# Kernel tuning notes

Measured on AMD Instinct MI355X. Metric: run time of the kernel, lower is better.

Reference implementation:

```python
import jax, jax.numpy as jnp
import numpy as np

T, N, L_DIM, P_DIM = 8192, 4096, 64, 32
IN_DIM = 3 * L_DIM  # library = [identity, square, sin]
MIN_TEMP, ALPHA, REP_COEF = 0.01, 0.999, 0.1


def build_library(X):
    # (T, L) -> (T, 3L): concatenated library features
    return jnp.concatenate([X, X * X, jnp.sin(X)], axis=1)


def setup_inputs() -> dict:
    key = jax.random.key(0)
    k = jax.random.split(key, 8)
    u = jax.random.uniform(k[6], (P_DIM, IN_DIM), minval=1e-7, maxval=1.0)
    return {
        "X_tilde_t_batch": jax.random.normal(k[0], (T, L_DIM), jnp.float32),
        "X_train_t_batch": jax.random.normal(k[1], (T, N), jnp.float32),
        "Y_train_t_batch": jax.random.normal(k[2], (T, N), jnp.float32),
        "temp": jnp.ones((1,), jnp.float32),
        "phi_bar_t": jax.random.normal(k[3], (P_DIM, L_DIM), jnp.float32) * 0.01,
        # spectral radius ~0.9 so the 8192-step linear recurrence stays bounded
        "A_tilde": jax.random.normal(k[4], (L_DIM, L_DIM), jnp.float32) * (0.9 / np.sqrt(L_DIM)),
        "U_l": jax.random.normal(k[5], (N, L_DIM), jnp.float32) / np.sqrt(N),
        "logits": jax.random.normal(k[7], (P_DIM, IN_DIM), jnp.float32),
        "gumbel_g": -jnp.log(-jnp.log(u)),  # Gumbel(0,1) noise, precomputed
    }


def reference(X_tilde_t_batch, X_train_t_batch, Y_train_t_batch, temp,
              phi_bar_t, A_tilde, U_l, logits, gumbel_g):
    # --- GumbelSelector (train=True) ---
    X_mod = build_library(X_tilde_t_batch)                           # (T, 3L)
    new_temp = jnp.maximum(MIN_TEMP, temp[0] * ALPHA)
    soft = jax.nn.softmax((logits + gumbel_g) / new_temp, axis=-1)   # (P, 3L)
    X_sel = X_mod @ soft.T                                           # (T, P) -- computed but unused downstream, as in source
    selected_idx = jnp.argmax(logits, axis=-1)                       # (P,)
    probs = jax.nn.softmax(logits, axis=-1)
    l0_pen = REP_COEF * jnp.sum(jnp.max(probs, axis=-1))             # computed, unused (as in source)

    # --- reconstruction_error: sequential linear state-space recurrence ---
    x0 = X_train_t_batch[0]                                          # (N,)  first column of X_train_batch
    xh0 = U_l.T @ x0                                                 # (L,)  projected initial state
    phi_bar = phi_bar_t.T                                            # (L, P)

    def step(xh, _):
        mod_sel = jnp.take(xh, selected_idx, mode='clip')            # (P,) irregular gather (clip matches jit take)
        xh = A_tilde @ xh + phi_bar @ mod_sel                        # tiny matvecs
        return xh, xh

    _, xh_seq = jax.lax.scan(step, xh0, None, length=T)              # (T, L)
    X_rec = xh_seq @ U_l.T                                           # (T, N) == (U_r @ xh_seq.T).T with U_r = U_l
    # Frobenius norm is transpose-invariant, so compute in (T, N) layout
    err = jnp.linalg.norm(Y_train_t_batch - X_rec) / jnp.linalg.norm(Y_train_t_batch)
    return (X_rec, err, new_temp, selected_idx)
```

## Files before the change

kernel.cpp:

```cpp
#include <hip/hip_runtime.h>
#include <math.h>

#define T_DIM 8192
#define N_DIM 4096
#define L 64
#define P 32
#define IN_DIM 192
#define S_CHUNK 16
#define N_CHUNK (T_DIM / S_CHUNK)
#define LDST 68

using f32x4   = __attribute__((ext_vector_type(4))) float;
using bf16x8  = __attribute__((ext_vector_type(8))) short;
using ushort8 = __attribute__((ext_vector_type(8))) unsigned short;

__device__ __forceinline__ unsigned short f2bf(float x) {
  unsigned u = __float_as_uint(x);
  u += 0x7fffu + ((u >> 16) & 1u);
  return (unsigned short)(u >> 16);
}
__device__ __forceinline__ float bf2f(unsigned short h) {
  return __uint_as_float(((unsigned)h) << 16);
}

__device__ __forceinline__ bf16x8 ldfrag(const unsigned short* __restrict__ base,
                                         int tile16, int gb, int lg, int lr) {
  return *(const bf16x8*)(base + ((size_t)((tile16 * 16 + gb + lg) * 16 + lr)) * 8);
}

__global__ __launch_bounds__(64) void k_xh0_part(const float* __restrict__ U,
                                                 const float* __restrict__ Xtr,
                                                 float* __restrict__ part,
                                                 double* __restrict__ acc) {
  int b = blockIdx.x;
  int l = threadIdx.x;
  if (b == 0 && l < 2) acc[l] = 0.0;
  int n0 = b * 64;
  float s = 0.f;
  #pragma unroll 8
  for (int i = 0; i < 64; ++i) {
    float x = Xtr[n0 + i];
    s += U[(size_t)(n0 + i) * L + l] * x;
  }
  part[b * 64 + l] = s;
}

__global__ __launch_bounds__(256) void k_usplit(const float* __restrict__ U,
                                                unsigned short* __restrict__ upk) {
  int idx = blockIdx.x * 256 + threadIdx.x;
  int lr = idx & 15, g = (idx >> 4) & 15, nn16 = idx >> 8;
  int n = nn16 * 16 + lr;
  int k0 = (g & 7) * 8;
  float4 a = *(const float4*)(U + (size_t)n * L + k0);
  float4 b = *(const float4*)(U + (size_t)n * L + k0 + 4);
  ushort8 o;
  float v[8] = {a.x, a.y, a.z, a.w, b.x, b.y, b.z, b.w};
  #pragma unroll
  for (int j = 0; j < 8; ++j) {
    unsigned short h = f2bf(v[j]);
    o[j] = (g < 8) ? h : f2bf(v[j] - bf2f(h));
  }
  *(ushort8*)(upk + (size_t)idx * 8) = o;
}

__global__ __launch_bounds__(256, 1) void k_prep(const float* __restrict__ A_tilde,
                                                 const float* __restrict__ phi_bar_t,
                                                 const float* __restrict__ logits,
                                                 const float* __restrict__ temp,
                                                 const float* __restrict__ part,
                                                 float* __restrict__ Wm,
                                                 float* __restrict__ xh0,
                                                 float* __restrict__ out_tail) {
  __shared__ float buf[2][64 * LDST];
  __shared__ float sphi[P * L];
  __shared__ float spart[4 * 64];
  __shared__ int   sel_s[P];
  int tid = threadIdx.x;

  #pragma unroll
  for (int i = 0; i < 4; ++i) {
    int f = tid + 256 * i;
    int r = f >> 4, q = f & 15;
    float4 v = ((const float4*)A_tilde)[f];
    *(float4*)(buf[0] + r * LDST + q * 4) = v;
  }
  #pragma unroll
  for (int i = 0; i < 2; ++i) {
    int f = tid + 256 * i;
    ((float4*)sphi)[f] = ((const float4*)phi_bar_t)[f];
  }
  {
    int l = tid & 63, q = tid >> 6;
    float s = 0.f;
    #pragma unroll
    for (int i = 0; i < 16; ++i)
      s += part[(q * 16 + i) * 64 + l];
    spart[q * 64 + l] = s;
  }
  {
    int p = tid >> 3, d = tid & 7;
    const float* row = logits + p * IN_DIM;
    float best = -1e30f; int bk = 0;
    #pragma unroll
    for (int j = 0; j < 6; ++j) {
      int kb = (j * 8 + d) * 4;
      float4 v = *(const float4*)(row + kb);
      if (v.x > best) { best = v.x; bk = kb; }
      if (v.y > best) { best = v.y; bk = kb + 1; }
      if (v.z > best) { best = v.z; bk = kb + 2; }
      if (v.w > best) { best = v.w; bk = kb + 3; }
    }
    #pragma unroll
    for (int off = 4; off > 0; off >>= 1) {
      float vo = __shfl_down(best, off, 8);
      int   ko = __shfl_down(bk,   off, 8);
      if (vo > best || (vo == best && ko < bk)) { best = vo; bk = ko; }
    }
    if (d == 0) {
      sel_s[p] = bk;
      out_tail[2 + p] = (float)bk;
    }
  }
  if (tid == 255) out_tail[1] = fmaxf(0.01f, temp[0] * 0.999f);
  __syncthreads();

  if (tid < L) {
    #pragma unroll 4
    for (int p = 0; p < P; ++p) {
      int kk = sel_s[p]; if (kk > L - 1) kk = L - 1;
      buf[0][tid * LDST + kk] += sphi[p * L + tid];
    }
  } else if (tid < 128) {
    int l = tid - 64;
    xh0[l] = spart[l] + spart[64 + l] + spart[128 + l] + spart[192 + l];
  }
  __syncthreads();

  #pragma unroll
  for (int i = 0; i < 4; ++i) {
    int f = tid + 256 * i;
    int r = f >> 4, q = f & 15;
    *(float4*)(Wm + r * 64 + q * 4) = *(const float4*)(buf[0] + r * LDST + q * 4);
  }

  int r0 = (tid >> 4) << 2;
  int c0 = (tid & 15) << 2;
  int cur = 0;
  for (int j = 1; j <= 12; ++j) {
    const float* S = buf[cur];
    float* D = buf[cur ^ 1];
    float acc[4][4];
    #pragma unroll
    for (int i = 0; i < 4; ++i)
      #pragma unroll
      for (int c = 0; c < 4; ++c) acc[i][c] = 0.f;

    #pragma unroll
    for (int kb = 0; kb < 64; kb += 16) {
      float a[4][16];
      #pragma unroll
      for (int i = 0; i < 4; ++i)
        #pragma unroll
        for (int q = 0; q < 4; ++q) {
          float4 t4 = *(const float4*)(S + (r0 + i) * LDST + kb + q * 4);
          a[i][q * 4 + 0] = t4.x; a[i][q * 4 + 1] = t4.y;
          a[i][q * 4 + 2] = t4.z; a[i][q * 4 + 3] = t4.w;
        }
      #pragma unroll
      for (int kk = 0; kk < 16; ++kk) {
        float4 b4 = *(const float4*)(S + (kb + kk) * LDST + c0);
        #pragma unroll
        for (int i = 0; i < 4; ++i) {
          acc[i][0] += a[i][kk] * b4.x;
          acc[i][1] += a[i][kk] * b4.y;
          acc[i][2] += a[i][kk] * b4.z;
          acc[i][3] += a[i][kk] * b4.w;
        }
      }
    }
    #pragma unroll
    for (int i = 0; i < 4; ++i) {
      float4 o = {acc[i][0], acc[i][1], acc[i][2], acc[i][3]};
      *(float4*)(D + (r0 + i) * LDST + c0) = o;
      *(float4*)(Wm + j * 4096 + (r0 + i) * 64 + c0) = o;
    }
    __syncthreads();
    cur ^= 1;
  }
}

__global__ __launch_bounds__(64) void k_states(const float* __restrict__ Wm,
                                               const float* __restrict__ xh0,
                                               unsigned short* __restrict__ xpk) {
  __shared__ float sx[16 * LDST];
  int c = blockIdx.x;
  int l = threadIdx.x;
  float v = xh0[l];
  int e = c << 4;
  for (int j = 4; j <= 12; ++j) {
    if ((e >> j) & 1) {
      const float* W = Wm + j * 4096;
      float n0 = 0.f, n1 = 0.f, n2 = 0.f, n3 = 0.f;
      #pragma unroll
      for (int k = 0; k < 64; k += 4) {
        n0 += W[l * 64 + k]     * __shfl(v, k, 64);
        n1 += W[l * 64 + k + 1] * __shfl(v, k + 1, 64);
        n2 += W[l * 64 + k + 2] * __shfl(v, k + 2, 64);
        n3 += W[l * 64 + k + 3] * __shfl(v, k + 3, 64);
      }
      v = (n0 + n1) + (n2 + n3);
    }
  }
  float m[64];
  #pragma unroll
  for (int k = 0; k < 64; ++k) m[k] = Wm[l * 64 + k];
  for (int i = 0; i < S_CHUNK; ++i) {
    float n0 = 0.f, n1 = 0.f, n2 = 0.f, n3 = 0.f;
    #pragma unroll
    for (int k = 0; k < 64; k += 4) {
      n0 += m[k]     * __shfl(v, k, 64);
      n1 += m[k + 1] * __shfl(v, k + 1, 64);
      n2 += m[k + 2] * __shfl(v, k + 2, 64);
      n3 += m[k + 3] * __shfl(v, k + 3, 64);
    }
    v = (n0 + n1) + (n2 + n3);
    sx[i * LDST + l] = v;
  }
  __syncthreads();

  #pragma unroll
  for (int it = 0; it < 4; ++it) {
    int idx = l + 64 * it;
    int lr = idx & 15, g = idx >> 4;
    int k0 = (g & 7) * 8;
    float4 a = *(const float4*)(sx + lr * LDST + k0);
    float4 b = *(const float4*)(sx + lr * LDST + k0 + 4);
    float vv[8] = {a.x, a.y, a.z, a.w, b.x, b.y, b.z, b.w};
    ushort8 o;
    #pragma unroll
    for (int j = 0; j < 8; ++j) {
      unsigned short h = f2bf(vv[j]);
      o[j] = (g < 8) ? h : f2bf(vv[j] - bf2f(h));
    }
    *(ushort8*)(xpk + ((size_t)c * 256 + idx) * 8) = o;
  }
}

__global__ __launch_bounds__(256, 3) void k_xrec(const unsigned short* __restrict__ xpk,
                                                 const unsigned short* __restrict__ upk,
                                                 const float* __restrict__ Y,
                                                 float* __restrict__ Xrec,
                                                 double* __restrict__ acc_g) {
  __shared__ float red[512];

  int tid = threadIdx.x;
  int nt = blockIdx.x & 31, tt = blockIdx.x >> 5;
  int n0 = nt * 128, t0 = tt * 128;

  int l = tid & 63, wid = tid >> 6;
  int wr = wid >> 1, wc = wid & 1;
  int lr = l & 15, lg = l >> 4;

  int xt = (t0 >> 4) + wr * 4;
  int un = (n0 >> 4) + wc * 4;

  f32x4 acc[4][4];
  #pragma unroll
  for (int m = 0; m < 4; ++m)
    #pragma unroll
    for (int nf = 0; nf < 4; ++nf) acc[m][nf] = (f32x4){0.f, 0.f, 0.f, 0.f};

  bf16x8 af[4], bfr[4], bf2r[4];

  #pragma unroll
  for (int m = 0; m < 4; ++m)  af[m]   = ldfrag(xpk, xt + m, 0, lg, lr);
  #pragma unroll
  for (int nf = 0; nf < 4; ++nf) bfr[nf]  = ldfrag(upk, un + nf, 0, lg, lr);
  #pragma unroll
  for (int nf = 0; nf < 4; ++nf) bf2r[nf] = ldfrag(upk, un + nf, 8, lg, lr);
  #pragma unroll
  for (int m = 0; m < 4; ++m)
    #pragma unroll
    for (int nf = 0; nf < 4; ++nf)
      acc[m][nf] = __builtin_amdgcn_mfma_f32_16x16x32_bf16(bfr[nf], af[m], acc[m][nf], 0, 0, 0);
  #pragma unroll
  for (int m = 0; m < 4; ++m)
    #pragma unroll
    for (int nf = 0; nf < 4; ++nf)
      acc[m][nf] = __builtin_amdgcn_mfma_f32_16x16x32_bf16(bf2r[nf], af[m], acc[m][nf], 0, 0, 0);

  #pragma unroll
  for (int m = 0; m < 4; ++m)  af[m]   = ldfrag(xpk, xt + m, 4, lg, lr);
  #pragma unroll
  for (int nf = 0; nf < 4; ++nf) bfr[nf]  = ldfrag(upk, un + nf, 4, lg, lr);
  #pragma unroll
  for (int nf = 0; nf < 4; ++nf) bf2r[nf] = ldfrag(upk, un + nf, 12, lg, lr);
  #pragma unroll
  for (int m = 0; m < 4; ++m)
    #pragma unroll
    for (int nf = 0; nf < 4; ++nf)
      acc[m][nf] = __builtin_amdgcn_mfma_f32_16x16x32_bf16(bfr[nf], af[m], acc[m][nf], 0, 0, 0);
  #pragma unroll
  for (int m = 0; m < 4; ++m)
    #pragma unroll
    for (int nf = 0; nf < 4; ++nf)
      acc[m][nf] = __builtin_amdgcn_mfma_f32_16x16x32_bf16(bf2r[nf], af[m], acc[m][nf], 0, 0, 0);

  #pragma unroll
  for (int m = 0; m < 4; ++m)  af[m]  = ldfrag(xpk, xt + m, 8, lg, lr);
  #pragma unroll
  for (int nf = 0; nf < 4; ++nf) bfr[nf] = ldfrag(upk, un + nf, 0, lg, lr);
  #pragma unroll
  for (int m = 0; m < 4; ++m)
    #pragma unroll
    for (int nf = 0; nf < 4; ++nf)
      acc[m][nf] = __builtin_amdgcn_mfma_f32_16x16x32_bf16(bfr[nf], af[m], acc[m][nf], 0, 0, 0);

  #pragma unroll
  for (int m = 0; m < 4; ++m)  af[m]  = ldfrag(xpk, xt + m, 12, lg, lr);
  #pragma unroll
  for (int nf = 0; nf < 4; ++nf) bfr[nf] = ldfrag(upk, un + nf, 4, lg, lr);
  #pragma unroll
  for (int m = 0; m < 4; ++m)
    #pragma unroll
    for (int nf = 0; nf < 4; ++nf)
      acc[m][nf] = __builtin_amdgcn_mfma_f32_16x16x32_bf16(bfr[nf], af[m], acc[m][nf], 0, 0, 0);

  float sd = 0.f, sy = 0.f;
  #pragma unroll
  for (int m = 0; m < 4; ++m) {
    #pragma unroll
    for (int nf = 0; nf < 4; ++nf) {
      int t = t0 + wr * 64 + m * 16 + lr;
      int n = n0 + wc * 64 + nf * 16 + lg * 4;
      size_t idx = (size_t)t * N_DIM + n;
      float4 y = *(const float4*)(Y + idx);
      f32x4 v = acc[m][nf];
      float d;
      d = y.x - v[0]; sd += d * d; sy += y.x * y.x;
      d = y.y - v[1]; sd += d * d; sy += y.y * y.y;
      d = y.z - v[2]; sd += d * d; sy += y.z * y.z;
      d = y.w - v[3]; sd += d * d; sy += y.w * y.w;
      __builtin_nontemporal_store(v, (f32x4*)(Xrec + idx));
    }
  }

  red[tid] = sd; red[256 + tid] = sy;
  __syncthreads();
  for (int s2 = 128; s2 > 0; s2 >>= 1) {
    if (tid < s2) { red[tid] += red[tid + s2]; red[256 + tid] += red[256 + tid + s2]; }
    __syncthreads();
  }
  if (tid == 0) {
    atomicAdd(acc_g,     (double)red[0]);
    atomicAdd(acc_g + 1, (double)red[256]);
  }
}

__global__ void k_err(const double* __restrict__ acc, float* __restrict__ out_tail) {
  out_tail[0] = (float)sqrt(acc[0] / acc[1]);
}

extern "C" void kernel_launch(void* const* d_in, const int* in_sizes, int n_in,
                              void* d_out, int out_size, void* d_ws, size_t ws_size,
                              hipStream_t stream) {
  const float* X_train = (const float*)d_in[1];
  const float* Y       = (const float*)d_in[2];
  const float* temp    = (const float*)d_in[3];
  const float* phi     = (const float*)d_in[4];
  const float* A_tilde = (const float*)d_in[5];
  const float* U       = (const float*)d_in[6];
  const float* logits  = (const float*)d_in[7];
  float* out = (float*)d_out;
  float* out_tail = out + (size_t)T_DIM * N_DIM;

  char* w = (char*)d_ws;
  double* acc          = (double*)w;
  float* Wm            = (float*)(w + 64);
  float* xh0           = (float*)(w + 213056);
  float* part          = (float*)(w + 213312);
  unsigned short* upk  = (unsigned short*)(w + 262144);
  unsigned short* xpk  = (unsigned short*)(w + 1310720);

  k_xh0_part<<<64, 64, 0, stream>>>(U, X_train, part, acc);
  k_usplit<<<(N_DIM / 16), 256, 0, stream>>>(U, upk);
  k_prep<<<1, 256, 0, stream>>>(A_tilde, phi, logits, temp, part, Wm, xh0, out_tail);
  k_states<<<N_CHUNK, 64, 0, stream>>>(Wm, xh0, xpk);
  k_xrec<<<2048, 256, 0, stream>>>(xpk, upk, Y, out, acc);
  k_err<<<1, 1, 0, stream>>>(acc, out_tail);
}
```

Baseline: 128.4 us.

## Retile X_rec GEMM to 16-row strips, merge init kernels, fold error into last block

Merges the xh0 partial-sum and U bf16-split kernels into one launch. Folds the final error computation into the X_rec kernel using a completion counter and last-block pattern, which removes two launches. Rewrites the X_rec GEMM so each block handles a 16-row time strip across half of N. Each wave keeps its A fragments in registers, streams U fragments through a loop, and writes with plain stores instead of nontemporal ones. This lowers register pressure so occupancy can go from 3 to 4 waves per SIMD, at the cost of reloading U fragments many times from cache.

```diff
diff --git a/kernel.cpp b/kernel.cpp
--- a/kernel.cpp
+++ b/kernel.cpp
@@ -28,39 +28,44 @@
   return *(const bf16x8*)(base + ((size_t)((tile16 * 16 + gb + lg) * 16 + lr)) * 8);
 }
 
-__global__ __launch_bounds__(64) void k_xh0_part(const float* __restrict__ U,
-                                                 const float* __restrict__ Xtr,
-                                                 float* __restrict__ part,
-                                                 double* __restrict__ acc) {
-  int b = blockIdx.x;
-  int l = threadIdx.x;
-  if (b == 0 && l < 2) acc[l] = 0.0;
-  int n0 = b * 64;
-  float s = 0.f;
-  #pragma unroll 8
-  for (int i = 0; i < 64; ++i) {
-    float x = Xtr[n0 + i];
-    s += U[(size_t)(n0 + i) * L + l] * x;
-  }
-  part[b * 64 + l] = s;
-}
-
-__global__ __launch_bounds__(256) void k_usplit(const float* __restrict__ U,
-                                                unsigned short* __restrict__ upk) {
-  int idx = blockIdx.x * 256 + threadIdx.x;
-  int lr = idx & 15, g = (idx >> 4) & 15, nn16 = idx >> 8;
-  int n = nn16 * 16 + lr;
-  int k0 = (g & 7) * 8;
-  float4 a = *(const float4*)(U + (size_t)n * L + k0);
-  float4 b = *(const float4*)(U + (size_t)n * L + k0 + 4);
-  ushort8 o;
-  float v[8] = {a.x, a.y, a.z, a.w, b.x, b.y, b.z, b.w};
-  #pragma unroll
-  for (int j = 0; j < 8; ++j) {
-    unsigned short h = f2bf(v[j]);
-    o[j] = (g < 8) ? h : f2bf(v[j] - bf2f(h));
-  }
-  *(ushort8*)(upk + (size_t)idx * 8) = o;
+__global__ __launch_bounds__(256) void k_init(const float* __restrict__ U,
+                                              const float* __restrict__ Xtr,
+                                              float* __restrict__ part,
+                                              double* __restrict__ acc,
+                                              int* __restrict__ cnt,
+                                              unsigned short* __restrict__ upk) {
+  int blk = blockIdx.x, tid = threadIdx.x;
+  if (blk < 16) {
+    if (blk == 0) {
+      if (tid < 2) acc[tid] = 0.0;
+      if (tid == 2) *cnt = 0;
+    }
+    int b = blk * 4 + (tid >> 6);
+    int l = tid & 63;
+    int n0 = b * 64;
+    float s = 0.f;
+    #pragma unroll 8
+    for (int i = 0; i < 64; ++i) {
+      float x = Xtr[n0 + i];
+      s += U[(size_t)(n0 + i) * L + l] * x;
+    }
+    part[b * 64 + l] = s;
+  } else {
+    int idx = (blk - 16) * 256 + tid;
+    int lr = idx & 15, g = (idx >> 4) & 15, nn16 = idx >> 8;
+    int n = nn16 * 16 + lr;
+    int k0 = (g & 7) * 8;
+    float4 a = *(const float4*)(U + (size_t)n * L + k0);
+    float4 b = *(const float4*)(U + (size_t)n * L + k0 + 4);
+    ushort8 o;
+    float v[8] = {a.x, a.y, a.z, a.w, b.x, b.y, b.z, b.w};
+    #pragma unroll
+    for (int j = 0; j < 8; ++j) {
+      unsigned short h = f2bf(v[j]);
+      o[j] = (g < 8) ? h : f2bf(v[j] - bf2f(h));
+    }
+    *(ushort8*)(upk + (size_t)idx * 8) = o;
+  }
 }
 
 __global__ __launch_bounds__(256, 1) void k_prep(const float* __restrict__ A_tilde,
@@ -246,103 +251,72 @@
   }
 }
 
-__global__ __launch_bounds__(256, 3) void k_xrec(const unsigned short* __restrict__ xpk,
+__global__ __launch_bounds__(256, 4) void k_xrec(const unsigned short* __restrict__ xpk,
                                                  const unsigned short* __restrict__ upk,
                                                  const float* __restrict__ Y,
                                                  float* __restrict__ Xrec,
-                                                 double* __restrict__ acc_g) {
+                                                 double* __restrict__ acc_g,
+                                                 int* __restrict__ cnt,
+                                                 float* __restrict__ out_tail) {
   __shared__ float red[512];
-
   int tid = threadIdx.x;
-  int nt = blockIdx.x & 31, tt = blockIdx.x >> 5;
-  int n0 = nt * 128, t0 = tt * 128;
-
-  int l = tid & 63, wid = tid >> 6;
-  int wr = wid >> 1, wc = wid & 1;
+  int raw = blockIdx.x;
+  int wg = (raw & 7) * 128 + (raw >> 3);
+  int th = wg >> 1;
+  int nh = wg & 1;
+  int t0 = th * 16;
+  int l = tid & 63, w = tid >> 6;
   int lr = l & 15, lg = l >> 4;
-
-  int xt = (t0 >> 4) + wr * 4;
-  int un = (n0 >> 4) + wc * 4;
-
-  f32x4 acc[4][4];
-  #pragma unroll
-  for (int m = 0; m < 4; ++m)
-    #pragma unroll
-    for (int nf = 0; nf < 4; ++nf) acc[m][nf] = (f32x4){0.f, 0.f, 0.f, 0.f};
-
-  bf16x8 af[4], bfr[4], bf2r[4];
-
-  #pragma unroll
-  for (int m = 0; m < 4; ++m)  af[m]   = ldfrag(xpk, xt + m, 0, lg, lr);
-  #pragma unroll
-  for (int nf = 0; nf < 4; ++nf) bfr[nf]  = ldfrag(upk, un + nf, 0, lg, lr);
-  #pragma unroll
-  for (int nf = 0; nf < 4; ++nf) bf2r[nf] = ldfrag(upk, un + nf, 8, lg, lr);
-  #pragma unroll
-  for (int m = 0; m < 4; ++m)
-    #pragma unroll
-    for (int nf = 0; nf < 4; ++nf)
-      acc[m][nf] = __builtin_amdgcn_mfma_f32_16x16x32_bf16(bfr[nf], af[m], acc[m][nf], 0, 0, 0);
-  #pragma unroll
-  for (int m = 0; m < 4; ++m)
-    #pragma unroll
-    for (int nf = 0; nf < 4; ++nf)
-      acc[m][nf] = __builtin_amdgcn_mfma_f32_16x16x32_bf16(bf2r[nf], af[m], acc[m][nf], 0, 0, 0);
-
-  #pragma unroll
-  for (int m = 0; m < 4; ++m)  af[m]   = ldfrag(xpk, xt + m, 4, lg, lr);
-  #pragma unroll
-  for (int nf = 0; nf < 4; ++nf) bfr[nf]  = ldfrag(upk, un + nf, 4, lg, lr);
-  #pragma unroll
-  for (int nf = 0; nf < 4; ++nf) bf2r[nf] = ldfrag(upk, un + nf, 12, lg, lr);
-  #pragma unroll
-  for (int m = 0; m < 4; ++m)
-    #pragma unroll
-    for (int nf = 0; nf < 4; ++nf)
-      acc[m][nf] = __builtin_amdgcn_mfma_f32_16x16x32_bf16(bfr[nf], af[m], acc[m][nf], 0, 0, 0);
-  #pragma unroll
-  for (int m = 0; m < 4; ++m)
-    #pragma unroll
-    for (int nf = 0; nf < 4; ++nf)
-      acc[m][nf] = __builtin_amdgcn_mfma_f32_16x16x32_bf16(bf2r[nf], af[m], acc[m][nf], 0, 0, 0);
-
-  #pragma unroll
-  for (int m = 0; m < 4; ++m)  af[m]  = ldfrag(xpk, xt + m, 8, lg, lr);
-  #pragma unroll
-  for (int nf = 0; nf < 4; ++nf) bfr[nf] = ldfrag(upk, un + nf, 0, lg, lr);
-  #pragma unroll
-  for (int m = 0; m < 4; ++m)
-    #pragma unroll
-    for (int nf = 0; nf < 4; ++nf)
-      acc[m][nf] = __builtin_amdgcn_mfma_f32_16x16x32_bf16(bfr[nf], af[m], acc[m][nf], 0, 0, 0);
-
-  #pragma unroll
-  for (int m = 0; m < 4; ++m)  af[m]  = ldfrag(xpk, xt + m, 12, lg, lr);
-  #pragma unroll
-  for (int nf = 0; nf < 4; ++nf) bfr[nf] = ldfrag(upk, un + nf, 4, lg, lr);
-  #pragma unroll
-  for (int m = 0; m < 4; ++m)
-    #pragma unroll
-    for (int nf = 0; nf < 4; ++nf)
-      acc[m][nf] = __builtin_amdgcn_mfma_f32_16x16x32_bf16(bfr[nf], af[m], acc[m][nf], 0, 0, 0);
+  int nwb = nh * 2048 + w * 512;
+
+  bf16x8 a_hi0 = ldfrag(xpk, th, 0,  lg, lr);
+  bf16x8 a_hi1 = ldfrag(xpk, th, 4,  lg, lr);
+  bf16x8 a_lo0 = ldfrag(xpk, th, 8,  lg, lr);
+  bf16x8 a_lo1 = ldfrag(xpk, th, 12, lg, lr);
 
   float sd = 0.f, sy = 0.f;
-  #pragma unroll
-  for (int m = 0; m < 4; ++m) {
-    #pragma unroll
-    for (int nf = 0; nf < 4; ++nf) {
-      int t = t0 + wr * 64 + m * 16 + lr;
-      int n = n0 + wc * 64 + nf * 16 + lg * 4;
-      size_t idx = (size_t)t * N_DIM + n;
-      float4 y = *(const float4*)(Y + idx);
-      f32x4 v = acc[m][nf];
-      float d;
-      d = y.x - v[0]; sd += d * d; sy += y.x * y.x;
-      d = y.y - v[1]; sd += d * d; sy += y.y * y.y;
-      d = y.z - v[2]; sd += d * d; sy += y.z * y.z;
-      d = y.w - v[3]; sd += d * d; sy += y.w * y.w;
-      __builtin_nontemporal_store(v, (f32x4*)(Xrec + idx));
-    }
+  int t = t0 + lr;
+  for (int g = 0; g < 16; ++g) {
+    int nf0 = (nwb >> 4) + g * 2;
+    bf16x8 u00 = ldfrag(upk, nf0,     0,  lg, lr);
+    bf16x8 u01 = ldfrag(upk, nf0,     4,  lg, lr);
+    bf16x8 u02 = ldfrag(upk, nf0,     8,  lg, lr);
+    bf16x8 u03 = ldfrag(upk, nf0,     12, lg, lr);
+    bf16x8 u10 = ldfrag(upk, nf0 + 1, 0,  lg, lr);
+    bf16x8 u11 = ldfrag(upk, nf0 + 1, 4,  lg, lr);
+    bf16x8 u12 = ldfrag(upk, nf0 + 1, 8,  lg, lr);
+    bf16x8 u13 = ldfrag(upk, nf0 + 1, 12, lg, lr);
+
+    size_t idx = (size_t)t * N_DIM + nwb + g * 32 + lg * 4;
+    float4 y0 = *(const float4*)(Y + idx);
+    float4 y1 = *(const float4*)(Y + idx + 16);
+
+    f32x4 acc0 = (f32x4){0.f, 0.f, 0.f, 0.f};
+    f32x4 acc1 = (f32x4){0.f, 0.f, 0.f, 0.f};
+    acc0 = __builtin_amdgcn_mfma_f32_16x16x32_bf16(u00, a_hi0, acc0, 0, 0, 0);
+    acc1 = __builtin_amdgcn_mfma_f32_16x16x32_bf16(u10, a_hi0, acc1, 0, 0, 0);
+    acc0 = __builtin_amdgcn_mfma_f32_16x16x32_bf16(u01, a_hi1, acc0, 0, 0, 0);
+    acc1 = __builtin_amdgcn_mfma_f32_16x16x32_bf16(u11, a_hi1, acc1, 0, 0, 0);
+    acc0 = __builtin_amdgcn_mfma_f32_16x16x32_bf16(u00, a_lo0, acc0, 0, 0, 0);
+    acc1 = __builtin_amdgcn_mfma_f32_16x16x32_bf16(u10, a_lo0, acc1, 0, 0, 0);
+    acc0 = __builtin_amdgcn_mfma_f32_16x16x32_bf16(u01, a_lo1, acc0, 0, 0, 0);
+    acc1 = __builtin_amdgcn_mfma_f32_16x16x32_bf16(u11, a_lo1, acc1, 0, 0, 0);
+    acc0 = __builtin_amdgcn_mfma_f32_16x16x32_bf16(u02, a_hi0, acc0, 0, 0, 0);
+    acc1 = __builtin_amdgcn_mfma_f32_16x16x32_bf16(u12, a_hi0, acc1, 0, 0, 0);
+    acc0 = __builtin_amdgcn_mfma_f32_16x16x32_bf16(u03, a_hi1, acc0, 0, 0, 0);
+    acc1 = __builtin_amdgcn_mfma_f32_16x16x32_bf16(u13, a_hi1, acc1, 0, 0, 0);
+
+    float d;
+    d = y0.x - acc0[0]; sd += d * d; sy += y0.x * y0.x;
+    d = y0.y - acc0[1]; sd += d * d; sy += y0.y * y0.y;
+    d = y0.z - acc0[2]; sd += d * d; sy += y0.z * y0.z;
+    d = y0.w - acc0[3]; sd += d * d; sy += y0.w * y0.w;
+    d = y1.x - acc1[0]; sd += d * d; sy += y1.x * y1.x;
+    d = y1.y - acc1[1]; sd += d * d; sy += y1.y * y1.y;
+    d = y1.z - acc1[2]; sd += d * d; sy += y1.z * y1.z;
+    d = y1.w - acc1[3]; sd += d * d; sy += y1.w * y1.w;
+    *(f32x4*)(Xrec + idx) = acc0;
+    *(f32x4*)(Xrec + idx + 16) = acc1;
   }
 
   red[tid] = sd; red[256 + tid] = sy;
@@ -354,11 +328,14 @@
   if (tid == 0) {
     atomicAdd(acc_g,     (double)red[0]);
     atomicAdd(acc_g + 1, (double)red[256]);
-  }
-}
-
-__global__ void k_err(const double* __restrict__ acc, float* __restrict__ out_tail) {
-  out_tail[0] = (float)sqrt(acc[0] / acc[1]);
+    __threadfence();
+    int done = atomicAdd(cnt, 1);
+    if (done == 1023) {
+      double s0 = atomicAdd(acc_g, 0.0);
+      double s1 = atomicAdd(acc_g + 1, 0.0);
+      out_tail[0] = (float)sqrt(s0 / s1);
+    }
+  }
 }
 
 extern "C" void kernel_launch(void* const* d_in, const int* in_sizes, int n_in,
@@ -376,16 +353,15 @@
 
   char* w = (char*)d_ws;
   double* acc          = (double*)w;
+  int* cnt             = (int*)(w + 32);
   float* Wm            = (float*)(w + 64);
   float* xh0           = (float*)(w + 213056);
   float* part          = (float*)(w + 213312);
   unsigned short* upk  = (unsigned short*)(w + 262144);
   unsigned short* xpk  = (unsigned short*)(w + 1310720);
 
-  k_xh0_part<<<64, 64, 0, stream>>>(U, X_train, part, acc);
-  k_usplit<<<(N_DIM / 16), 256, 0, stream>>>(U, upk);
+  k_init<<<272, 256, 0, stream>>>(U, X_train, part, acc, cnt, upk);
   k_prep<<<1, 256, 0, stream>>>(A_tilde, phi, logits, temp, part, Wm, xh0, out_tail);
   k_states<<<N_CHUNK, 64, 0, stream>>>(Wm, xh0, xpk);
-  k_xrec<<<2048, 256, 0, stream>>>(xpk, upk, Y, out, acc);
-  k_err<<<1, 1, 0, stream>>>(acc, out_tail);
-}
+  k_xrec<<<1024, 256, 0, stream>>>(xpk, upk, Y, out, acc, cnt, out_tail);
+}
```

After: 177.6 us. 1.38x slower.
